# Kernel optimization log

Hardware: AMD Instinct MI355X
Metric: run time of the kernel (lower is better)

Reference implementation:

```python
import jax, jax.numpy as jnp
import numpy as np
import math

# tcnn HashGrid config (instant-ngp defaults, Smoothstep interpolation)
N_LEVELS = 16
F_PER_LEVEL = 2
LOG2_T = 19
T = 1 << LOG2_T            # hashmap size per level
BASE_RES = 16
PER_LEVEL_SCALE = 2.0
PRIMES = (1, 2654435761)   # tcnn spatial hash primes for 2D
IN_DIM = 2

# 4 corner offsets of the 2D cell, tcnn ordering (dim0 fastest)
_OFFSETS = jnp.array([[0, 0], [1, 0], [0, 1], [1, 1]], dtype=jnp.int32)  # [4,2]


def setup_inputs() -> dict:
    key = jax.random.key(0)
    k1, k2 = jax.random.split(key)
    # atlas coords in [-1, 1] as the wrapper expects (it maps to [0,1])
    x = jax.random.uniform(k1, (64, 64, 128, IN_DIM), jnp.float32, -1.0, 1.0)
    # tcnn initializes hash tables uniform in [-1e-4, 1e-4]
    table = jax.random.uniform(k2, (N_LEVELS, T, F_PER_LEVEL), jnp.float32, -1e-4, 1e-4)
    return {"x": x, "table": table}


def _encode(x01, table):
    # x01: [N, 2] in [0, 1]; table: [L, T, F]
    outs = []
    for l in range(N_LEVELS):
        # grid_scale = exp2(level * log2(per_level_scale)) * base_resolution - 1
        scale = (PER_LEVEL_SCALE ** l) * BASE_RES - 1.0
        res = int(math.ceil(scale)) + 1
        pos = x01 * jnp.float32(scale) + 0.5
        pg = jnp.floor(pos)
        frac = pos - pg                       # [N,2]
        pg = pg.astype(jnp.int32)
        # Smoothstep interpolation weights
        w = frac * frac * (3.0 - 2.0 * frac)  # [N,2]
        corners = pg[:, None, :] + _OFFSETS[None]                     # [N,4,2]
        cw = jnp.where(_OFFSETS[None].astype(bool),
                       w[:, None, :], 1.0 - w[:, None, :]).prod(-1)   # [N,4]
        if res * res <= T:
            # dense (non-hashed) level: row-major index, wrapped like tcnn
            idx = (corners[..., 0] + corners[..., 1] * res) % (res * res)
        else:
            cu = corners.astype(jnp.uint32)
            h = (cu[..., 0] * jnp.uint32(PRIMES[0])) ^ (cu[..., 1] * jnp.uint32(PRIMES[1]))
            idx = (h & jnp.uint32(T - 1)).astype(jnp.int32)
        feats = table[l][idx]                                         # [N,4,F]
        outs.append((cw[..., None] * feats).sum(axis=1))              # [N,F]
    return jnp.concatenate(outs, axis=-1)                             # [N, L*F]


def reference(x, table):
    Nv, Nr, Nm, C = x.shape
    x01 = x.reshape(-1, C) * 0.5 + 0.5
    enc = _encode(x01, table)
    return enc.reshape(Nv, Nr, Nm, -1)
```

## Files before the change

### kernel.cpp

```cpp
#include <hip/hip_runtime.h>
#include <stdint.h>


#define HG_LEVELS 16
#define HG_T (1u << 19)
#define HG_PRIME1 2654435761u

__global__ __launch_bounds__(256) void hashgrid_encode_kernel(
    const float2* __restrict__ x,
    const float* __restrict__ table,
    float* __restrict__ out,
    int npts)
{
    int i = blockIdx.x * blockDim.x + threadIdx.x;
    if (i >= npts) return;

    float2 xi = x[i];
    float x0 = xi.x * 0.5f + 0.5f;
    float x1 = xi.y * 0.5f + 0.5f;

    float acc[2 * HG_LEVELS];

#pragma unroll
    for (int l = 0; l < HG_LEVELS; ++l) {
        const int res = 16 << l;
        const float scale = (float)res - 1.0f;
        const bool dense = (l <= 5);

        float p0 = x0 * scale + 0.5f;
        float p1 = x1 * scale + 0.5f;
        float g0 = floorf(p0);
        float g1 = floorf(p1);
        float fr0 = p0 - g0;
        float fr1 = p1 - g1;
        uint32_t c0 = (uint32_t)(int)g0;
        uint32_t c1 = (uint32_t)(int)g1;

        float w0 = fr0 * fr0 * (3.0f - 2.0f * fr0);
        float w1 = fr1 * fr1 * (3.0f - 2.0f * fr1);

        uint32_t i00, i10, i01, i11;
        if (dense) {
            const uint32_t mask = (uint32_t)res * (uint32_t)res - 1u;
            uint32_t r0 = c0;
            uint32_t r1 = c0 + 1u;
            uint32_t b0 = c1 * (uint32_t)res;
            uint32_t b1 = (c1 + 1u) * (uint32_t)res;
            i00 = (r0 + b0) & mask;
            i10 = (r1 + b0) & mask;
            i01 = (r0 + b1) & mask;
            i11 = (r1 + b1) & mask;
        } else {
            uint32_t h0 = c1 * HG_PRIME1;
            uint32_t h1 = (c1 + 1u) * HG_PRIME1;
            i00 = (c0 ^ h0) & (HG_T - 1u);
            i10 = ((c0 + 1u) ^ h0) & (HG_T - 1u);
            i01 = (c0 ^ h1) & (HG_T - 1u);
            i11 = ((c0 + 1u) ^ h1) & (HG_T - 1u);
        }

        const float* tl = table + (size_t)l * (size_t)HG_T * 2u;
        float2 f00 = *(const float2*)(tl + (size_t)i00 * 2u);
        float2 f10 = *(const float2*)(tl + (size_t)i10 * 2u);
        float2 f01 = *(const float2*)(tl + (size_t)i01 * 2u);
        float2 f11 = *(const float2*)(tl + (size_t)i11 * 2u);

        float w00 = (1.0f - w0) * (1.0f - w1);
        float w10 = w0 * (1.0f - w1);
        float w01 = (1.0f - w0) * w1;
        float w11 = w0 * w1;

        acc[2 * l + 0] = w00 * f00.x + w10 * f10.x + w01 * f01.x + w11 * f11.x;
        acc[2 * l + 1] = w00 * f00.y + w10 * f10.y + w01 * f01.y + w11 * f11.y;
    }

    float4* o = (float4*)(out + (size_t)i * (2 * HG_LEVELS));
#pragma unroll
    for (int j = 0; j < 8; ++j) {
        o[j] = make_float4(acc[4 * j + 0], acc[4 * j + 1], acc[4 * j + 2], acc[4 * j + 3]);
    }
}

extern "C" void kernel_launch(void* const* d_in, const int* in_sizes, int n_in,
                              void* d_out, int out_size, void* d_ws, size_t ws_size,
                              hipStream_t stream) {
    const float2* x = (const float2*)d_in[0];
    const float* table = (const float*)d_in[1];
    float* out = (float*)d_out;

    int npts = in_sizes[0] / 2;
    int block = 256;
    int grid = (npts + block - 1) / block;
    hashgrid_encode_kernel<<<grid, block, 0, stream>>>(x, table, out, npts);
}
```

Before: 303.3 us.

## Process two points per thread and add per-level block barriers for gather locality

Each thread now encodes two points, loading their coordinates as one float4 and issuing both points' eight gathers per level together to raise memory-level parallelism. A __syncthreads is inserted after each hashed level so threads in a block stay in lockstep on the same level's table, likely to improve L2 locality across the 4MB per-level tables. Costs include doubled accumulator registers, which lowers occupancy, plus barrier stalls; odd point counts are not handled, and out-of-range threads are clamped to the last pair and write it redundantly.

New measurement: 266.6 us. -12.1%, faster.

```diff
diff --git a/kernel.cpp b/kernel.cpp
--- a/kernel.cpp
+++ b/kernel.cpp
@@ -6,90 +6,114 @@
 #define HG_T (1u << 19)
 #define HG_PRIME1 2654435761u
 
-__global__ __launch_bounds__(256) void hashgrid_encode_kernel(
-    const float2* __restrict__ x,
+__device__ __forceinline__ void level_setup(float x0, float x1, int l,
+                                            uint32_t idx[4], float w[4])
+{
+    const int res = 16 << l;
+    const float scale = (float)res - 1.0f;
+    float p0 = x0 * scale + 0.5f;
+    float p1 = x1 * scale + 0.5f;
+    float g0 = floorf(p0);
+    float g1 = floorf(p1);
+    float fr0 = p0 - g0;
+    float fr1 = p1 - g1;
+    uint32_t c0 = (uint32_t)(int)g0;
+    uint32_t c1 = (uint32_t)(int)g1;
+    float w0 = fr0 * fr0 * (3.0f - 2.0f * fr0);
+    float w1 = fr1 * fr1 * (3.0f - 2.0f * fr1);
+
+    if (l <= 5) {
+        const uint32_t mask = (uint32_t)res * (uint32_t)res - 1u;
+        uint32_t b0 = c1 * (uint32_t)res;
+        uint32_t b1 = (c1 + 1u) * (uint32_t)res;
+        idx[0] = (c0 + b0) & mask;
+        idx[1] = (c0 + 1u + b0) & mask;
+        idx[2] = (c0 + b1) & mask;
+        idx[3] = (c0 + 1u + b1) & mask;
+    } else {
+        uint32_t h0 = c1 * HG_PRIME1;
+        uint32_t h1 = (c1 + 1u) * HG_PRIME1;
+        idx[0] = (c0 ^ h0) & (HG_T - 1u);
+        idx[1] = ((c0 + 1u) ^ h0) & (HG_T - 1u);
+        idx[2] = (c0 ^ h1) & (HG_T - 1u);
+        idx[3] = ((c0 + 1u) ^ h1) & (HG_T - 1u);
+    }
+    w[0] = (1.0f - w0) * (1.0f - w1);
+    w[1] = w0 * (1.0f - w1);
+    w[2] = (1.0f - w0) * w1;
+    w[3] = w0 * w1;
+}
+
+__global__ __launch_bounds__(256) void hashgrid_encode2_kernel(
+    const float4* __restrict__ x,
     const float* __restrict__ table,
     float* __restrict__ out,
-    int npts)
+    int npairs)
 {
-    int i = blockIdx.x * blockDim.x + threadIdx.x;
-    if (i >= npts) return;
+    int t = blockIdx.x * blockDim.x + threadIdx.x;
+    if (t >= npairs) t = npairs - 1;
 
-    float2 xi = x[i];
-    float x0 = xi.x * 0.5f + 0.5f;
-    float x1 = xi.y * 0.5f + 0.5f;
+    float4 xp = x[t];
+    float a0 = xp.x * 0.5f + 0.5f;
+    float a1 = xp.y * 0.5f + 0.5f;
+    float b0 = xp.z * 0.5f + 0.5f;
+    float b1 = xp.w * 0.5f + 0.5f;
 
-    float acc[2 * HG_LEVELS];
+    float accA[2 * HG_LEVELS];
+    float accB[2 * HG_LEVELS];
 
 #pragma unroll
     for (int l = 0; l < HG_LEVELS; ++l) {
-        const int res = 16 << l;
-        const float scale = (float)res - 1.0f;
-        const bool dense = (l <= 5);
+        uint32_t ia[4], ib[4];
+        float wa[4], wb[4];
+        level_setup(a0, a1, l, ia, wa);
+        level_setup(b0, b1, l, ib, wb);
 
-        float p0 = x0 * scale + 0.5f;
-        float p1 = x1 * scale + 0.5f;
-        float g0 = floorf(p0);
-        float g1 = floorf(p1);
-        float fr0 = p0 - g0;
-        float fr1 = p1 - g1;
-        uint32_t c0 = (uint32_t)(int)g0;
-        uint32_t c1 = (uint32_t)(int)g1;
+        const float2* tl = (const float2*)(table + (size_t)l * (size_t)HG_T * 2u);
+        float2 fa[4], fb[4];
+#pragma unroll
+        for (int c = 0; c < 4; ++c) fa[c] = tl[ia[c]];
+#pragma unroll
+        for (int c = 0; c < 4; ++c) fb[c] = tl[ib[c]];
 
-        float w0 = fr0 * fr0 * (3.0f - 2.0f * fr0);
-        float w1 = fr1 * fr1 * (3.0f - 2.0f * fr1);
+        float sAx = 0.f, sAy = 0.f, sBx = 0.f, sBy = 0.f;
+#pragma unroll
+        for (int c = 0; c < 4; ++c) {
+            sAx += wa[c] * fa[c].x;
+            sAy += wa[c] * fa[c].y;
+            sBx += wb[c] * fb[c].x;
+            sBy += wb[c] * fb[c].y;
+        }
+        accA[2 * l + 0] = sAx;
+        accA[2 * l + 1] = sAy;
+        accB[2 * l + 0] = sBx;
+        accB[2 * l + 1] = sBy;
 
-        uint32_t i00, i10, i01, i11;
-        if (dense) {
-            const uint32_t mask = (uint32_t)res * (uint32_t)res - 1u;
-            uint32_t r0 = c0;
-            uint32_t r1 = c0 + 1u;
-            uint32_t b0 = c1 * (uint32_t)res;
-            uint32_t b1 = (c1 + 1u) * (uint32_t)res;
-            i00 = (r0 + b0) & mask;
-            i10 = (r1 + b0) & mask;
-            i01 = (r0 + b1) & mask;
-            i11 = (r1 + b1) & mask;
-        } else {
-            uint32_t h0 = c1 * HG_PRIME1;
-            uint32_t h1 = (c1 + 1u) * HG_PRIME1;
-            i00 = (c0 ^ h0) & (HG_T - 1u);
-            i10 = ((c0 + 1u) ^ h0) & (HG_T - 1u);
-            i01 = (c0 ^ h1) & (HG_T - 1u);
-            i11 = ((c0 + 1u) ^ h1) & (HG_T - 1u);
-        }
-
-        const float* tl = table + (size_t)l * (size_t)HG_T * 2u;
-        float2 f00 = *(const float2*)(tl + (size_t)i00 * 2u);
-        float2 f10 = *(const float2*)(tl + (size_t)i10 * 2u);
-        float2 f01 = *(const float2*)(tl + (size_t)i01 * 2u);
-        float2 f11 = *(const float2*)(tl + (size_t)i11 * 2u);
-
-        float w00 = (1.0f - w0) * (1.0f - w1);
-        float w10 = w0 * (1.0f - w1);
-        float w01 = (1.0f - w0) * w1;
-        float w11 = w0 * w1;
-
-        acc[2 * l + 0] = w00 * f00.x + w10 * f10.x + w01 * f01.x + w11 * f11.x;
-        acc[2 * l + 1] = w00 * f00.y + w10 * f10.y + w01 * f01.y + w11 * f11.y;
+        if (l >= 5 && l < HG_LEVELS - 1) __syncthreads();
     }
 
-    float4* o = (float4*)(out + (size_t)i * (2 * HG_LEVELS));
+    float4* oA = (float4*)(out + (size_t)(2 * t + 0) * (2 * HG_LEVELS));
+    float4* oB = (float4*)(out + (size_t)(2 * t + 1) * (2 * HG_LEVELS));
 #pragma unroll
-    for (int j = 0; j < 8; ++j) {
-        o[j] = make_float4(acc[4 * j + 0], acc[4 * j + 1], acc[4 * j + 2], acc[4 * j + 3]);
-    }
+    for (int j = 0; j < 8; ++j)
+        oA[j] = make_float4(accA[4 * j + 0], accA[4 * j + 1],
+                            accA[4 * j + 2], accA[4 * j + 3]);
+#pragma unroll
+    for (int j = 0; j < 8; ++j)
+        oB[j] = make_float4(accB[4 * j + 0], accB[4 * j + 1],
+                            accB[4 * j + 2], accB[4 * j + 3]);
 }
 
 extern "C" void kernel_launch(void* const* d_in, const int* in_sizes, int n_in,
                               void* d_out, int out_size, void* d_ws, size_t ws_size,
                               hipStream_t stream) {
-    const float2* x = (const float2*)d_in[0];
+    const float4* x = (const float4*)d_in[0];
     const float* table = (const float*)d_in[1];
     float* out = (float*)d_out;
 
     int npts = in_sizes[0] / 2;
+    int npairs = npts / 2;
     int block = 256;
-    int grid = (npts + block - 1) / block;
-    hashgrid_encode_kernel<<<grid, block, 0, stream>>>(x, table, out, npts);
+    int grid = (npairs + block - 1) / block;
+    hashgrid_encode2_kernel<<<grid, block, 0, stream>>>(x, table, out, npairs);
 }
```

## Add per-level block barriers and nontemporal I/O to hashgrid encoder

Applied to the files above, without the earlier changes.

Places a __syncthreads after each hashed level so the waves in a block move through the levels together, which keeps each level's gather working set localized in cache. The input loads and output stores become nontemporal so the streaming data does not evict table lines. Out-of-range threads are clamped instead of returning, which the barriers require; those threads recompute the last point and rewrite its output. Launch bounds now request 4 blocks per CU. The barriers add synchronization stalls in exchange for better cache reuse.

Result: slower. 325.9 us (+7.4%).

```diff
diff --git a/kernel.cpp b/kernel.cpp
--- a/kernel.cpp
+++ b/kernel.cpp
@@ -6,16 +6,19 @@
 #define HG_T (1u << 19)
 #define HG_PRIME1 2654435761u
 
-__global__ __launch_bounds__(256) void hashgrid_encode_kernel(
-    const float2* __restrict__ x,
+typedef float vfloat2 __attribute__((ext_vector_type(2)));
+typedef float vfloat4 __attribute__((ext_vector_type(4)));
+
+__global__ __launch_bounds__(256, 4) void hashgrid_encode5_kernel(
+    const float* __restrict__ x,
     const float* __restrict__ table,
     float* __restrict__ out,
     int npts)
 {
     int i = blockIdx.x * blockDim.x + threadIdx.x;
-    if (i >= npts) return;
+    if (i >= npts) i = npts - 1;
 
-    float2 xi = x[i];
+    vfloat2 xi = __builtin_nontemporal_load((const vfloat2*)(x + 2 * (size_t)i));
     float x0 = xi.x * 0.5f + 0.5f;
     float x1 = xi.y * 0.5f + 0.5f;
 
@@ -25,8 +28,6 @@
     for (int l = 0; l < HG_LEVELS; ++l) {
         const int res = 16 << l;
         const float scale = (float)res - 1.0f;
-        const bool dense = (l <= 5);
-
         float p0 = x0 * scale + 0.5f;
         float p1 = x1 * scale + 0.5f;
         float g0 = floorf(p0);
@@ -35,21 +36,18 @@
         float fr1 = p1 - g1;
         uint32_t c0 = (uint32_t)(int)g0;
         uint32_t c1 = (uint32_t)(int)g1;
-
         float w0 = fr0 * fr0 * (3.0f - 2.0f * fr0);
         float w1 = fr1 * fr1 * (3.0f - 2.0f * fr1);
 
         uint32_t i00, i10, i01, i11;
-        if (dense) {
+        if (l <= 5) {
             const uint32_t mask = (uint32_t)res * (uint32_t)res - 1u;
-            uint32_t r0 = c0;
-            uint32_t r1 = c0 + 1u;
             uint32_t b0 = c1 * (uint32_t)res;
             uint32_t b1 = (c1 + 1u) * (uint32_t)res;
-            i00 = (r0 + b0) & mask;
-            i10 = (r1 + b0) & mask;
-            i01 = (r0 + b1) & mask;
-            i11 = (r1 + b1) & mask;
+            i00 = (c0 + b0) & mask;
+            i10 = (c0 + 1u + b0) & mask;
+            i01 = (c0 + b1) & mask;
+            i11 = (c0 + 1u + b1) & mask;
         } else {
             uint32_t h0 = c1 * HG_PRIME1;
             uint32_t h1 = (c1 + 1u) * HG_PRIME1;
@@ -59,11 +57,11 @@
             i11 = ((c0 + 1u) ^ h1) & (HG_T - 1u);
         }
 
-        const float* tl = table + (size_t)l * (size_t)HG_T * 2u;
-        float2 f00 = *(const float2*)(tl + (size_t)i00 * 2u);
-        float2 f10 = *(const float2*)(tl + (size_t)i10 * 2u);
-        float2 f01 = *(const float2*)(tl + (size_t)i01 * 2u);
-        float2 f11 = *(const float2*)(tl + (size_t)i11 * 2u);
+        const float2* tl = (const float2*)(table + (size_t)l * (size_t)HG_T * 2u);
+        float2 f00 = tl[i00];
+        float2 f10 = tl[i10];
+        float2 f01 = tl[i01];
+        float2 f11 = tl[i11];
 
         float w00 = (1.0f - w0) * (1.0f - w1);
         float w10 = w0 * (1.0f - w1);
@@ -72,24 +70,28 @@
 
         acc[2 * l + 0] = w00 * f00.x + w10 * f10.x + w01 * f01.x + w11 * f11.x;
         acc[2 * l + 1] = w00 * f00.y + w10 * f10.y + w01 * f01.y + w11 * f11.y;
+
+        if (l >= 5 && l < HG_LEVELS - 1) __syncthreads();
     }
 
-    float4* o = (float4*)(out + (size_t)i * (2 * HG_LEVELS));
+    float* o = out + (size_t)i * (2 * HG_LEVELS);
 #pragma unroll
     for (int j = 0; j < 8; ++j) {
-        o[j] = make_float4(acc[4 * j + 0], acc[4 * j + 1], acc[4 * j + 2], acc[4 * j + 3]);
+        vfloat4 v = { acc[4 * j + 0], acc[4 * j + 1],
+                      acc[4 * j + 2], acc[4 * j + 3] };
+        __builtin_nontemporal_store(v, (vfloat4*)(o + 4 * j));
     }
 }
 
 extern "C" void kernel_launch(void* const* d_in, const int* in_sizes, int n_in,
                               void* d_out, int out_size, void* d_ws, size_t ws_size,
                               hipStream_t stream) {
-    const float2* x = (const float2*)d_in[0];
+    const float* x = (const float*)d_in[0];
     const float* table = (const float*)d_in[1];
     float* out = (float*)d_out;
 
     int npts = in_sizes[0] / 2;
     int block = 256;
     int grid = (npts + block - 1) / block;
-    hashgrid_encode_kernel<<<grid, block, 0, stream>>>(x, table, out, npts);
+    hashgrid_encode5_kernel<<<grid, block, 0, stream>>>(x, table, out, npts);
 }
```
